# Optimization experiments

Hardware: AMD Instinct MI355X
Metric: run time of the kernel (lower is better)

## Reference

```python
import jax, jax.numpy as jnp
import numpy as np

B, C, W, H, NH, FF, L = 4, 200, 300, 128, 8, 512, 2
PH = H // NH
MAXLEN = 200
PE_N = 512
NEG = -1e15


def _sinusoidal_pe():
    # fairseq-style sinusoidal table, get_embedding(512, hidden_size)
    half = H // 2
    freq = np.exp(np.arange(half, dtype=np.float64) * -(np.log(10000.0) / (half - 1)))
    ang = np.arange(PE_N, dtype=np.float64)[:, None] * freq[None, :]
    return jnp.asarray(np.concatenate([np.sin(ang), np.cos(ang)], axis=1), jnp.float32)

PE = _sinusoidal_pe()  # [512, H], frozen (requires_grad=False in torch)


def setup_inputs() -> dict:
    key = jax.random.key(0)
    ks = jax.random.split(key, 20)

    def lin(k, fan_in, shape):
        lim = 1.0 / np.sqrt(fan_in)
        return jax.random.uniform(k, shape, jnp.float32, -lim, lim)

    return {
        'chars': jax.random.normal(ks[0], (B, C, H), jnp.float32),
        'words': jax.random.normal(ks[1], (B, W, H), jnp.float32),
        'pos_s': jax.random.randint(ks[2], (B, C), 0, MAXLEN),
        'pos_e': jax.random.randint(ks[3], (B, C), 0, MAXLEN),
        'lex_s': jax.random.randint(ks[4], (B, W), 0, MAXLEN),
        'lex_e': jax.random.randint(ks[5], (B, W), 0, MAXLEN),
        'seq_len': jax.random.randint(ks[6], (B,), 100, C + 1),
        'lex_num': jax.random.randint(ks[7], (B,), 150, W + 1),
        # Four_Pos_Fusion 'ff': Linear(4H -> H) + ReLU
        'Wf': lin(ks[8], 4 * H, (4 * H, H)),
        'bf': jnp.zeros((H,), jnp.float32),
        # per-layer attention / FFN params, stacked on leading layer dim
        'Wq': lin(ks[9], H, (L, H, H)),  'bq': jnp.zeros((L, H), jnp.float32),
        'Wk': lin(ks[10], H, (L, H, H)), 'bk': jnp.zeros((L, H), jnp.float32),
        'Wv': lin(ks[11], H, (L, H, H)), 'bv': jnp.zeros((L, H), jnp.float32),
        'Wr': lin(ks[12], H, (L, H, H)), 'br': jnp.zeros((L, H), jnp.float32),
        'u_bias': jax.random.normal(ks[13], (L, NH, PH), jnp.float32) * 0.02,
        'v_bias': jax.random.normal(ks[14], (L, NH, PH), jnp.float32) * 0.02,
        'ln1_g': jnp.ones((L, H), jnp.float32), 'ln1_b': jnp.zeros((L, H), jnp.float32),
        'ln2_g': jnp.ones((L, H), jnp.float32), 'ln2_b': jnp.zeros((L, H), jnp.float32),
        'W1': lin(ks[15], H, (L, H, FF)),  'b1': jnp.zeros((L, FF), jnp.float32),
        'W2': lin(ks[16], FF, (L, FF, H)), 'b2': jnp.zeros((L, H), jnp.float32),
    }


def _ln(x, g, b):
    m = jnp.mean(x, -1, keepdims=True)
    v = jnp.var(x, -1, keepdims=True)
    return (x - m) / jnp.sqrt(v + 1e-5) * g + b


def reference(chars, words, pos_s, pos_e, lex_s, lex_e, seq_len, lex_num,
              Wf, bf, Wq, bq, Wk, bk, Wv, bv, Wr, br, u_bias, v_bias,
              ln1_g, ln1_b, ln2_g, ln2_b, W1, b1, W2, b2):
    # four relative-position distance tables (char span vs word span), offset by max_seq_len
    idx = lambda p, l: jnp.clip(p[:, :, None] - l[:, None, :] + MAXLEN, 0, PE_N - 1)
    # Linear(4H->H) over the concat of four gathered PE tensors, expressed as
    # a sum of 4 chunked matmuls to avoid materializing the [B,C,W,4H] concat.
    rel = (PE[idx(pos_s, lex_s)] @ Wf[0:H] + PE[idx(pos_s, lex_e)] @ Wf[H:2 * H]
           + PE[idx(pos_e, lex_s)] @ Wf[2 * H:3 * H] + PE[idx(pos_e, lex_e)] @ Wf[3 * H:4 * H] + bf)
    rel = jax.nn.relu(rel)  # [B, C, W, H]

    # char_lex_len_to_mask: valid (char i, word j) pairs
    mask = (jnp.arange(C) < seq_len[:, None])[:, :, None] & (jnp.arange(W) < lex_num[:, None])[:, None, :]
    mask = mask[:, None]  # [B, 1, C, W]

    out = chars
    for i in range(L):
        q = (out @ Wq[i] + bq[i]).reshape(B, C, NH, PH)
        k = (words @ Wk[i] + bk[i]).reshape(B, W, NH, PH)
        v = (words @ Wv[i] + bv[i]).reshape(B, W, NH, PH)
        r = (rel @ Wr[i] + br[i]).reshape(B, C, W, NH, PH)
        A_C = jnp.einsum('bcnp,bwnp->bncw', q + u_bias[i], k)
        B_D = jnp.einsum('bcnp,bcwnp->bncw', q + v_bias[i], r)
        score = jnp.where(mask, A_C + B_D, NEG)  # scale=False
        att = jax.nn.softmax(score, axis=-1)
        att = jnp.where(mask, att, 0.0)  # dropout=0 (eval)
        ctx = jnp.einsum('bncw,bwnp->bcnp', att, v).reshape(B, C, H)
        out = _ln(ctx + out, ln1_g[i], ln1_b[i])
        ff = jax.nn.relu(out @ W1[i] + b1[i]) @ W2[i] + b2[i]
        out = _ln(ff + out, ln2_g[i], ln2_b[i])
    return out
```

## Files before the change

kernel.cpp:

```cpp
#include <hip/hip_runtime.h>
#include <math.h>

#define B_ 4
#define C_ 200
#define CH_ 100
#define W_ 300
#define WP_ 304
#define H_ 128
#define NH_ 8
#define PH_ 16
#define FF_ 512
#define L_ 2
#define MAXLEN_ 200
#define PEN_ 512
#define WVS_ 136
#define NTILE_ 19

typedef __bf16 bf16x8 __attribute__((ext_vector_type(8)));
typedef float f32x4v __attribute__((ext_vector_type(4)));

#define SEG_PEW   64
#define SEG_KV    (SEG_PEW + 200)
#define SEG_WR    (SEG_KV + 256)
#define SEG_W1T   (SEG_WR + 128)
#define PREP_BLOCKS (SEG_W1T + 128)

__global__ __launch_bounds__(128) void prep_kernel(
        const float* __restrict__ Wf, const float* __restrict__ bfv,
        const float* __restrict__ words,
        const float* __restrict__ Wk, const float* __restrict__ bk,
        const float* __restrict__ Wv, const float* __restrict__ bv,
        const float* __restrict__ Wr, const float* __restrict__ W1,
        const float* __restrict__ W2,
        __bf16* __restrict__ kb, __bf16* __restrict__ PEWb, __bf16* __restrict__ vTb,
        __bf16* __restrict__ WrB, __bf16* __restrict__ W1T, __bf16* __restrict__ W2T) {
    __shared__ __align__(16) float s_buf[12 * H_];
    __shared__ __align__(16) __bf16 s_vt[128][12];
    __shared__ float s_tile[32][33];
// ... 95 lines not shown
        for (int k = 0; k < 8; ++k) {
            int j = jt * 32 + r + 4 * k;
            s_tile[r + 4 * k][cc] = W1[(l * H_ + j) * FF_ + ut * 32 + cc];
        }
        __syncthreads();
        int jl = t & 31, ul = t >> 5;
        #pragma unroll
        for (int k = 0; k < 8; ++k) {
            int u = ut * 32 + ul + 4 * k;
            W1T[((size_t)(l * FF_ + u)) * H_ + jt * 32 + jl] = (__bf16)s_tile[jl][ul + 4 * k];
        }
    } else {
        int blk = blockIdx.x - SEG_W1T;
        int l = blk >> 6;
        int rem = blk & 63;
        int ut = rem >> 2;
        int ht = rem & 3;
        int r = t >> 5, cc = t & 31;
        #pragma unroll
        for (int k = 0; k < 8; ++k) {
            int u = ut * 32 + r + 4 * k;
            s_tile[r + 4 * k][cc] = W2[(l * FF_ + u) * H_ + ht * 32 + cc];
        }
        __syncthreads();
        int ul = t & 31, hl = t >> 5;
        #pragma unroll
        for (int k = 0; k < 8; ++k) {
            int h = ht * 32 + hl + 4 * k;
            W2T[((size_t)(l * H_ + h)) * FF_ + ut * 32 + ul] = (__bf16)s_tile[ul][hl + 4 * k];
        }
    }
}

__global__ __launch_bounds__(256, 2) void mega_kernel(
    const float* __restrict__ chars,
    const int* __restrict__ pos_s, const int* __restrict__ pos_e,
    const int* __restrict__ lex_s, const int* __restrict__ lex_e,
    const int* __restrict__ seq_len, const int* __restrict__ lex_num,
    const float* __restrict__ Wq, const float* __restrict__ bq,
    const float* __restrict__ br,
    const float* __restrict__ u_bias, const float* __restrict__ v_bias,
    const float* __restrict__ ln1_g, const float* __restrict__ ln1_b,
    const float* __restrict__ ln2_g, const float* __restrict__ ln2_b,
    const float* __restrict__ b1, const float* __restrict__ b2,
    const __bf16* __restrict__ kb, const __bf16* __restrict__ PEWb,
    const __bf16* __restrict__ vTb, const __bf16* __restrict__ WrB,
    const __bf16* __restrict__ W1T, const __bf16* __restrict__ W2T,
    float* __restrict__ out) {

    __shared__ __align__(16) float s_x[2][H_], s_qv[2][H_];
    __shared__ __align__(16) __bf16 s_wvecb[2][16][WVS_];
    __shared__ __align__(16) __bf16 s_qub[2][16][WVS_];
    __shared__ float s_bterm[2][NH_];
    __shared__ __align__(16) float s_sc[2][NH_][WP_];
    __shared__ float s_red[2][132];
    __shared__ __align__(16) float s_hid[2][FF_];
    __shared__ float s_tmp[2][256];
    __shared__ int s_ls[W_], s_le[W_];

    int blk = blockIdx.x;
    int b = blk / CH_, c0 = blk % CH_;
    int t = threadIdx.x;
    int lane = t & 63;
    int wid = t >> 6;
    int l15 = lane & 15, quad = lane >> 4;

    if (t < H_) {
        s_x[0][t] = chars[(b * C_ + c0) * H_ + t];
        s_x[1][t] = chars[(b * C_ + c0 + CH_) * H_ + t];
    }
    for (int w = t; w < W_; w += 256) {
        s_ls[w] = lex_s[b * W_ + w];
        s_le[w] = lex_e[b * W_ + w];
    }
    for (int i = t; i < 2 * 8 * WVS_; i += 256) {
        int r = i / (8 * WVS_), rem = i % (8 * WVS_);
        s_wvecb[r][8 + rem / WVS_][rem % WVS_] = (__bf16)0.f;
    }
    for (int i = t; i < 2 * 16 * WVS_; i += 256) {
        int r = i / (16 * WVS_), rem = i % (16 * WVS_);
        s_qub[r][rem / WVS_][rem % WVS_] = (__bf16)0.f;
    }
    int ps0 = pos_s[b * C_ + c0],        pev0 = pos_e[b * C_ + c0];
    int ps1 = pos_s[b * C_ + c0 + CH_],  pev1 = pos_e[b * C_ + c0 + CH_];
    int slen = seq_len[b];
    int cvalid0 = (c0 < slen), cvalid1 = (c0 + CH_ < slen);
    int wnum = lex_num[b];
    __syncthreads();

    bf16x8 Ac0[5][4], Ac1[5][4];

    #pragma unroll
    for (int li = 0; li < L_; ++li) {
        {
            int half = t >> 7, h = t & 127;
            const float* WqL = Wq + li * H_ * H_;
            const float4* x40 = (const float4*)s_x[0];
            const float4* x41 = (const float4*)s_x[1];
            float4 a0 = {0,0,0,0}, a1 = {0,0,0,0};
            #pragma unroll 2
            for (int g = half * 16; g < half * 16 + 16; ++g) {
                float4 xa = x40[g], xb = x41[g];
                int j0 = 4 * g;
                float w0 = WqL[(j0 + 0) * H_ + h], w1 = WqL[(j0 + 1) * H_ + h];
                float w2 = WqL[(j0 + 2) * H_ + h], w3 = WqL[(j0 + 3) * H_ + h];
                a0.x += xa.x * w0; a0.y += xa.y * w1; a0.z += xa.z * w2; a0.w += xa.w * w3;
                a1.x += xb.x * w0; a1.y += xb.y * w1; a1.z += xb.z * w2; a1.w += xb.w * w3;
            }
            s_tmp[0][t] = (a0.x + a0.y) + (a0.z + a0.w);
            s_tmp[1][t] = (a1.x + a1.y) + (a1.z + a1.w);
        }
        __syncthreads();
        if (t < H_) {
            #pragma unroll
            for (int r = 0; r < 2; ++r) {
                float acc = s_tmp[r][t] + s_tmp[r][t + 128] + bq[li * H_ + t];
                s_qub[r][t >> 4][t] = (__bf16)(acc + u_bias[li * H_ + t]);
                s_qv[r][t] = acc + v_bias[li * H_ + t];
            }
        }
        __syncthreads();

        if (t < H_) {
            const __bf16* WrRow = WrB + li * H_ * H_ + t * H_;
            #pragma unroll 2
            for (int n = 0; n < NH_; ++n) {
                bf16x8 w0 = *(const bf16x8*)(WrRow + n * PH_);
                bf16x8 w1 = *(const bf16x8*)(WrRow + n * PH_ + 8);
                #pragma unroll
                for (int r = 0; r < 2; ++r) {
                    const float4* qv4 = (const float4*)(s_qv[r] + n * PH_);
                    float4 q0 = qv4[0], q1 = qv4[1], q2 = qv4[2], q3 = qv4[3];
                    float4 a4;
                    a4.x = (float)w0[0] * q0.x + (float)w1[0] * q2.x;
                    a4.y = (float)w0[1] * q0.y + (float)w1[1] * q2.y;
                    a4.z = (float)w0[2] * q0.z + (float)w1[2] * q2.z;
                    a4.w = (float)w0[3] * q0.w + (float)w1[3] * q2.w;
                    a4.x += (float)w0[4] * q1.x + (float)w1[4] * q3.x;
                    a4.y += (float)w0[5] * q1.y + (float)w1[5] * q3.y;
                    a4.z += (float)w0[6] * q1.z + (float)w1[6] * q3.z;
                    a4.w += (float)w0[7] * q1.w + (float)w1[7] * q3.w;
                    s_wvecb[r][n][t] = (__bf16)((a4.x + a4.y) + (a4.z + a4.w));
                }
            }
        } else if (t < H_ + NH_) {
            int n = t - H_;
            const float4* br4 = (const float4*)(br + li * H_ + n * PH_);
            float4 b0 = br4[0], b1v = br4[1], b2v = br4[2], b3v = br4[3];
            #pragma unroll
            for (int r = 0; r < 2; ++r) {
                const float4* qv4 = (const float4*)(s_qv[r] + n * PH_);
                float4 q0 = qv4[0], q1 = qv4[1], q2 = qv4[2], q3 = qv4[3];
                float4 a4;
                a4.x = b0.x * q0.x + b2v.x * q2.x;
                a4.y = b0.y * q0.y + b2v.y * q2.y;
                a4.z = b0.z * q0.z + b2v.z * q2.z;
                a4.w = b0.w * q0.w + b2v.w * q2.w;
                a4.x += b1v.x * q1.x + b3v.x * q3.x;
                a4.y += b1v.y * q1.y + b3v.y * q3.y;
                a4.z += b1v.z * q1.z + b3v.z * q3.z;
                a4.w += b1v.w * q1.w + b3v.w * q3.w;
                s_bterm[r][n] = (a4.x + a4.y) + (a4.z + a4.w);
            }
        }
        __syncthreads();

        const __bf16* kL = kb + (size_t)(li * B_ + b) * W_ * H_;
        {
            const __bf16* wrow0 = &s_wvecb[0][l15][0];
            const __bf16* wrow1 = &s_wvecb[1][l15][0];
            const __bf16* qrow0 = &s_qub[0][l15][0];
            const __bf16* qrow1 = &s_qub[1][l15][0];
            #pragma unroll
            for (int tc = 0; tc < 5; ++tc) {
                int tile = wid + 4 * tc;
                if (tile < NTILE_) {
                    int w0t = tile * 16;
                    int w = w0t + l15; if (w > W_ - 1) w = W_ - 1;
                    const __bf16* kr = kL + (size_t)w * H_;
                    f32x4v acc0 = {0.f,0.f,0.f,0.f}, acc1 = {0.f,0.f,0.f,0.f};
                    if (li == 0) {
                        int ls = s_ls[w], le = s_le[w];
                        int i00 = min(max(ps0 - ls + MAXLEN_, 0), PEN_ - 1);
                        int i01 = min(max(ps0 - le + MAXLEN_, 0), PEN_ - 1);
                        int i02 = min(max(pev0 - ls + MAXLEN_, 0), PEN_ - 1);
                        int i03 = min(max(pev0 - le + MAXLEN_, 0), PEN_ - 1);
                        int i10 = min(max(ps1 - ls + MAXLEN_, 0), PEN_ - 1);
                        int i11 = min(max(ps1 - le + MAXLEN_, 0), PEN_ - 1);
                        int i12 = min(max(pev1 - ls + MAXLEN_, 0), PEN_ - 1);
                        int i13 = min(max(pev1 - le + MAXLEN_, 0), PEN_ - 1);
                        const __bf16* r00 = PEWb + (size_t)(0 * PEN_ + i00) * H_;
                        const __bf16* r01 = PEWb + (size_t)(1 * PEN_ + i01) * H_;
                        const __bf16* r02 = PEWb + (size_t)(2 * PEN_ + i02) * H_;
                        const __bf16* r03 = PEWb + (size_t)(3 * PEN_ + i03) * H_;
                        const __bf16* r10 = PEWb + (size_t)(0 * PEN_ + i10) * H_;
                        const __bf16* r11 = PEWb + (size_t)(1 * PEN_ + i11) * H_;
                        const __bf16* r12 = PEWb + (size_t)(2 * PEN_ + i12) * H_;
                        const __bf16* r13 = PEWb + (size_t)(3 * PEN_ + i13) * H_;
                        #pragma unroll
                        for (int s = 0; s < 4; ++s) {
                            int h0 = s * 32 + quad * 8;
                            bf16x8 K = *(const bf16x8*)(kr + h0);
                            bf16x8 A0, A1;
                            {
                                bf16x8 t0 = *(const bf16x8*)(r00 + h0);
                                bf16x8 t1 = *(const bf16x8*)(r01 + h0);
                                bf16x8 t2 = *(const bf16x8*)(r02 + h0);
                                bf16x8 t3 = *(const bf16x8*)(r03 + h0);
                                #pragma unroll
                                for (int j = 0; j < 8; ++j)
                                    A0[j] = (__bf16)fmaxf((float)t0[j] + (float)t1[j] + (float)t2[j] + (float)t3[j], 0.f);
                            }
                            {
                                bf16x8 t0 = *(const bf16x8*)(r10 + h0);
                                bf16x8 t1 = *(const bf16x8*)(r11 + h0);
                                bf16x8 t2 = *(const bf16x8*)(r12 + h0);
                                bf16x8 t3 = *(const bf16x8*)(r13 + h0);
                                #pragma unroll
                                for (int j = 0; j < 8; ++j)
                                    A1[j] = (__bf16)fmaxf((float)t0[j] + (float)t1[j] + (float)t2[j] + (float)t3[j], 0.f);
                            }
                            Ac0[tc][s] = A0;
                            Ac1[tc][s] = A1;
                            bf16x8 Bf0 = *(const bf16x8*)(wrow0 + h0);
                            acc0 = __builtin_amdgcn_mfma_f32_16x16x32_bf16(A0, Bf0, acc0, 0, 0, 0);
                            bf16x8 Bq0 = *(const bf16x8*)(qrow0 + h0);
                            acc0 = __builtin_amdgcn_mfma_f32_16x16x32_bf16(K, Bq0, acc0, 0, 0, 0);
                            bf16x8 Bf1 = *(const bf16x8*)(wrow1 + h0);
                            acc1 = __builtin_amdgcn_mfma_f32_16x16x32_bf16(A1, Bf1, acc1, 0, 0, 0);
                            bf16x8 Bq1 = *(const bf16x8*)(qrow1 + h0);
                            acc1 = __builtin_amdgcn_mfma_f32_16x16x32_bf16(K, Bq1, acc1, 0, 0, 0);
                        }
                    } else {
                        #pragma unroll
                        for (int s = 0; s < 4; ++s) {
                            int h0 = s * 32 + quad * 8;
                            bf16x8 K = *(const bf16x8*)(kr + h0);
                            bf16x8 A0 = Ac0[tc][s];
                            bf16x8 A1 = Ac1[tc][s];
                            bf16x8 Bf0 = *(const bf16x8*)(wrow0 + h0);
                            acc0 = __builtin_amdgcn_mfma_f32_16x16x32_bf16(A0, Bf0, acc0, 0, 0, 0);
                            bf16x8 Bq0 = *(const bf16x8*)(qrow0 + h0);
                            acc0 = __builtin_amdgcn_mfma_f32_16x16x32_bf16(K, Bq0, acc0, 0, 0, 0);
                            bf16x8 Bf1 = *(const bf16x8*)(wrow1 + h0);
                            acc1 = __builtin_amdgcn_mfma_f32_16x16x32_bf16(A1, Bf1, acc1, 0, 0, 0);
                            bf16x8 Bq1 = *(const bf16x8*)(qrow1 + h0);
                            acc1 = __builtin_amdgcn_mfma_f32_16x16x32_bf16(K, Bq1, acc1, 0, 0, 0);
                        }
                    }
                    if (l15 < NH_) {
                        float bt0 = s_bterm[0][l15], bt1 = s_bterm[1][l15];
                        #pragma unroll
                        for (int r = 0; r < 4; ++r) {
                            int wr = w0t + quad * 4 + r;
                            if (wr < W_) {
                                s_sc[0][l15][wr] = acc0[r] + bt0;
                                s_sc[1][l15][wr] = acc1[r] + bt1;
                            }
                        }
                    }
                }
            }
        }
        __syncthreads();

        {
            int n = t >> 5, ln_ = t & 31;
            #pragma unroll
            for (int r = 0; r < 2; ++r) {
                int cval = r ? cvalid1 : cvalid0;
                if (cval) {
                    float m = -INFINITY;
                    for (int w = ln_; w < wnum; w += 32) m = fmaxf(m, s_sc[r][n][w]);
                    #pragma unroll
                    for (int off = 16; off > 0; off >>= 1) m = fmaxf(m, __shfl_xor(m, off, 32));
                    float sum = 0.f;
                    for (int w = ln_; w < wnum; w += 32) sum += expf(s_sc[r][n][w] - m);
                    #pragma unroll
                    for (int off = 16; off > 0; off >>= 1) sum += __shfl_xor(sum, off, 32);
                    float inv = 1.f / sum;
                    for (int w = ln_; w < WP_; w += 32)
                        s_sc[r][n][w] = (w < wnum) ? expf(s_sc[r][n][w] - m) * inv : 0.f;
                } else {
                    for (int w = ln_; w < WP_; w += 32) s_sc[r][n][w] = 0.f;
                }
            }
        }
        __syncthreads();

        {
            int h = t & 127, half = t >> 7, n = h >> 4;
            const __bf16* vrow = vTb + ((size_t)(li * B_ + b) * H_ + h) * WP_;
            const float4* att0 = (const float4*)(s_sc[0][n]);
            const float4* att1 = (const float4*)(s_sc[1][n]);
            float4 a0 = {0,0,0,0}, a1 = {0,0,0,0};
            #pragma unroll 2
            for (int g = half * 19; g < half * 19 + 19; ++g) {
                bf16x8 vv = *(const bf16x8*)(vrow + 8 * g);
                float4 p00 = att0[2 * g], p01 = att0[2 * g + 1];
                float4 p10 = att1[2 * g], p11 = att1[2 * g + 1];
                float v0 = (float)vv[0], v1 = (float)vv[1], v2 = (float)vv[2], v3 = (float)vv[3];
                float v4 = (float)vv[4], v5 = (float)vv[5], v6 = (float)vv[6], v7 = (float)vv[7];
                a0.x += p00.x * v0 + p01.x * v4;
                a0.y += p00.y * v1 + p01.y * v5;
                a0.z += p00.z * v2 + p01.z * v6;
                a0.w += p00.w * v3 + p01.w * v7;
                a1.x += p10.x * v0 + p11.x * v4;
                a1.y += p10.y * v1 + p11.y * v5;
                a1.z += p10.z * v2 + p11.z * v6;
                a1.w += p10.w * v3 + p11.w * v7;
            }
            s_tmp[0][t] = (a0.x + a0.y) + (a0.z + a0.w);
            s_tmp[1][t] = (a1.x + a1.y) + (a1.z + a1.w);
        }
        __syncthreads();

        if (t < 128) {
            s_red[0][t] = s_tmp[0][t] + s_tmp[0][t + 128] + s_x[0][t];
        } else {
            int e = t - 128;
            s_red[1][e] = s_tmp[1][e] + s_tmp[1][e + 128] + s_x[1][e];
        }
        __syncthreads();
        if (t < 128) {
            int r = t >> 6, l = t & 63;
            float a = s_red[r][l], bb = s_red[r][l + 64];
            float s = a + bb, ss = a * a + bb * bb;
            #pragma unroll
            for (int off = 32; off > 0; off >>= 1) {
                s += __shfl_down(s, off);
                ss += __shfl_down(ss, off);
            }
            if (l == 0) {
                float mean = s * (1.f / 128.f);
                float var = ss * (1.f / 128.f) - mean * mean;
                s_red[r][128] = mean;
                s_red[r][129] = rsqrtf(var + 1e-5f);
            }
        }
        __syncthreads();
        if (t < H_) {
            float g1 = ln1_g[li * H_ + t], b1v = ln1_b[li * H_ + t];
            #pragma unroll
            for (int r = 0; r < 2; ++r)
                s_x[r][t] = (s_red[r][t] - s_red[r][128]) * s_red[r][129] * g1 + b1v;
        }
        __syncthreads();

        {
            const __bf16* W1l = W1T + (size_t)li * FF_ * H_;
            int u0 = t * 2;
            const __bf16* ra = W1l + (size_t)u0 * H_;
            const __bf16* rb = W1l + (size_t)(u0 + 1) * H_;
            const float4* x40 = (const float4*)s_x[0];
            const float4* x41 = (const float4*)s_x[1];
            float4 a00 = {0,0,0,0}, a01 = {0,0,0,0}, a10 = {0,0,0,0}, a11 = {0,0,0,0};
            #pragma unroll 2
            for (int g = 0; g < 16; ++g) {
                bf16x8 wa = *(const bf16x8*)(ra + 8 * g);
                bf16x8 wb = *(const bf16x8*)(rb + 8 * g);
                float4 xa0 = x40[2 * g], xa1 = x40[2 * g + 1];
                float4 xb0 = x41[2 * g], xb1 = x41[2 * g + 1];
                a00.x += xa0.x * (float)wa[0] + xa1.x * (float)wa[4];
                a00.y += xa0.y * (float)wa[1] + xa1.y * (float)wa[5];
                a00.z += xa0.z * (float)wa[2] + xa1.z * (float)wa[6];
                a00.w += xa0.w * (float)wa[3] + xa1.w * (float)wa[7];
                a01.x += xa0.x * (float)wb[0] + xa1.x * (float)wb[4];
                a01.y += xa0.y * (float)wb[1] + xa1.y * (float)wb[5];
                a01.z += xa0.z * (float)wb[2] + xa1.z * (float)wb[6];
                a01.w += xa0.w * (float)wb[3] + xa1.w * (float)wb[7];
                a10.x += xb0.x * (float)wa[0] + xb1.x * (float)wa[4];
                a10.y += xb0.y * (float)wa[1] + xb1.y * (float)wa[5];
                a10.z += xb0.z * (float)wa[2] + xb1.z * (float)wa[6];
                a10.w += xb0.w * (float)wa[3] + xb1.w * (float)wa[7];
                a11.x += xb0.x * (float)wb[0] + xb1.x * (float)wb[4];
                a11.y += xb0.y * (float)wb[1] + xb1.y * (float)wb[5];
                a11.z += xb0.z * (float)wb[2] + xb1.z * (float)wb[6];
                a11.w += xb0.w * (float)wb[3] + xb1.w * (float)wb[7];
            }
            float bb0 = b1[li * FF_ + u0], bb1 = b1[li * FF_ + u0 + 1];
            s_hid[0][u0]     = fmaxf((a00.x + a00.y) + (a00.z + a00.w) + bb0, 0.f);
            s_hid[0][u0 + 1] = fmaxf((a01.x + a01.y) + (a01.z + a01.w) + bb1, 0.f);
            s_hid[1][u0]     = fmaxf((a10.x + a10.y) + (a10.z + a10.w) + bb0, 0.f);
            s_hid[1][u0 + 1] = fmaxf((a11.x + a11.y) + (a11.z + a11.w) + bb1, 0.f);
        }
        __syncthreads();

        {
            int half = t >> 7, h = t & 127;
            const __bf16* wrow2 = W2T + ((size_t)li * H_ + h) * FF_ + half * 256;
            const float4* h40 = (const float4*)(s_hid[0] + half * 256);
            const float4* h41 = (const float4*)(s_hid[1] + half * 256);
            float4 a0 = {0,0,0,0}, a1 = {0,0,0,0};
            #pragma unroll 2
            for (int g = 0; g < 32; ++g) {
                bf16x8 wv = *(const bf16x8*)(wrow2 + 8 * g);
                float4 p00 = h40[2 * g], p01 = h40[2 * g + 1];
                float4 p10 = h41[2 * g], p11 = h41[2 * g + 1];
                float v0 = (float)wv[0], v1 = (float)wv[1], v2 = (float)wv[2], v3 = (float)wv[3];
                float v4 = (float)wv[4], v5 = (float)wv[5], v6 = (float)wv[6], v7 = (float)wv[7];
                a0.x += p00.x * v0 + p01.x * v4;
                a0.y += p00.y * v1 + p01.y * v5;
                a0.z += p00.z * v2 + p01.z * v6;
                a0.w += p00.w * v3 + p01.w * v7;
                a1.x += p10.x * v0 + p11.x * v4;
                a1.y += p10.y * v1 + p11.y * v5;
                a1.z += p10.z * v2 + p11.z * v6;
                a1.w += p10.w * v3 + p11.w * v7;
            }
            s_tmp[0][t] = (a0.x + a0.y) + (a0.z + a0.w);
            s_tmp[1][t] = (a1.x + a1.y) + (a1.z + a1.w);
        }
        __syncthreads();

        if (t < 128) {
            s_red[0][t] = s_tmp[0][t] + s_tmp[0][t + 128] + b2[li * H_ + t] + s_x[0][t];
        } else {
            int e = t - 128;
            s_red[1][e] = s_tmp[1][e] + s_tmp[1][e + 128] + b2[li * H_ + e] + s_x[1][e];
        }
        __syncthreads();
        if (t < 128) {
            int r = t >> 6, l = t & 63;
            float a = s_red[r][l], bb = s_red[r][l + 64];
            float s = a + bb, ss = a * a + bb * bb;
            #pragma unroll
            for (int off = 32; off > 0; off >>= 1) {
                s += __shfl_down(s, off);
                ss += __shfl_down(ss, off);
            }
            if (l == 0) {
                float mean = s * (1.f / 128.f);
                float var = ss * (1.f / 128.f) - mean * mean;
                s_red[r][128] = mean;
                s_red[r][129] = rsqrtf(var + 1e-5f);
            }
        }
        __syncthreads();
        if (t < H_) {
            float g2 = ln2_g[li * H_ + t], b2v = ln2_b[li * H_ + t];
            #pragma unroll
            for (int r = 0; r < 2; ++r)
                s_x[r][t] = (s_red[r][t] - s_red[r][128]) * s_red[r][129] * g2 + b2v;
        }
        __syncthreads();
    }

    if (t < H_) {
        out[(b * C_ + c0) * H_ + t] = s_x[0][t];
        out[(b * C_ + c0 + CH_) * H_ + t] = s_x[1][t];
    }
}

extern "C" void kernel_launch(void* const* d_in, const int* in_sizes, int n_in,
                              void* d_out, int out_size, void* d_ws, size_t ws_size,
                              hipStream_t stream) {
    const float* chars  = (const float*)d_in[0];
    const float* words  = (const float*)d_in[1];
    const int* pos_s   = (const int*)d_in[2];
    const int* pos_e   = (const int*)d_in[3];
    const int* lex_s   = (const int*)d_in[4];
    const int* lex_e   = (const int*)d_in[5];
    const int* seq_len = (const int*)d_in[6];
    const int* lex_num = (const int*)d_in[7];
    const float* Wf  = (const float*)d_in[8];
    const float* bfv = (const float*)d_in[9];
    const float* Wq  = (const float*)d_in[10];
    const float* bq  = (const float*)d_in[11];
    const float* Wk  = (const float*)d_in[12];
    const float* bk  = (const float*)d_in[13];
    const float* Wv  = (const float*)d_in[14];
    const float* bv  = (const float*)d_in[15];
    const float* Wr  = (const float*)d_in[16];
    const float* br  = (const float*)d_in[17];
    const float* u_bias = (const float*)d_in[18];
    const float* v_bias = (const float*)d_in[19];
    const float* ln1_g  = (const float*)d_in[20];
    const float* ln1_b  = (const float*)d_in[21];
    const float* ln2_g  = (const float*)d_in[22];
    const float* ln2_b  = (const float*)d_in[23];
    const float* W1  = (const float*)d_in[24];
    const float* b1  = (const float*)d_in[25];
    const float* W2  = (const float*)d_in[26];
    const float* b2  = (const float*)d_in[27];

    __bf16* kb   = (__bf16*)d_ws;
    __bf16* PEWb = kb + (size_t)L_ * B_ * W_ * H_;
    __bf16* vTb  = PEWb + 4 * PEN_ * H_;
    __bf16* WrB  = vTb + (size_t)L_ * B_ * H_ * WP_;
    __bf16* W1T  = WrB + L_ * H_ * H_;
    __bf16* W2T  = W1T + L_ * H_ * FF_;

    prep_kernel<<<dim3(PREP_BLOCKS), dim3(128), 0, stream>>>(
        Wf, bfv, words, Wk, bk, Wv, bv, Wr, W1, W2,
        kb, PEWb, vTb, WrB, W1T, W2T);

    mega_kernel<<<dim3(B_ * CH_), dim3(256), 0, stream>>>(
        chars, pos_s, pos_e, lex_s, lex_e, seq_len, lex_num,
        Wq, bq, br, u_bias, v_bias,
        ln1_g, ln1_b, ln2_g, ln2_b, b1, b2,
        kb, PEWb, vTb, WrB, W1T, W2T, (float*)d_out);
}
```

Baseline: 245.3 us.

## Process four chars per block and recompute rel-pos A tiles each layer

Each block now handles four character rows instead of two, halving the grid to 200 blocks and reusing each loaded weight, key and PE row across four rows. Shared memory moves to a dynamic allocation of about 93 KB, and launch bounds drop to one block per SM. The register cache of layer-0 relative-position A fragments is removed, so the PE gather and ReLU sum are recomputed in every layer to free registers. The cost is fewer blocks for parallelism, since 200 blocks may underfill the GPU's compute units, plus redundant gather work in layer 1.

```diff
diff --git a/kernel.cpp b/kernel.cpp
--- a/kernel.cpp
+++ b/kernel.cpp
@@ -3,7 +3,8 @@
 
 #define B_ 4
 #define C_ 200
-#define CH_ 100
+#define CR_ 50
+#define NR_ 4
 #define W_ 300
 #define WP_ 304
 #define H_ 128
@@ -165,7 +166,8 @@
     }
 }
 
-__global__ __launch_bounds__(256, 2) void mega_kernel(
+#define SMEM_BYTES 94752
+__global__ __launch_bounds__(256, 1) void mega_kernel(
     const float* __restrict__ chars,
     const int* __restrict__ pos_s, const int* __restrict__ pos_e,
     const int* __restrict__ lex_s, const int* __restrict__ lex_e,
@@ -181,72 +183,83 @@
     const __bf16* __restrict__ W1T, const __bf16* __restrict__ W2T,
     float* __restrict__ out) {
 
-    __shared__ __align__(16) float s_x[2][H_], s_qv[2][H_];
-    __shared__ __align__(16) __bf16 s_wvecb[2][16][WVS_];
-    __shared__ __align__(16) __bf16 s_qub[2][16][WVS_];
-    __shared__ float s_bterm[2][NH_];
-    __shared__ __align__(16) float s_sc[2][NH_][WP_];
-    __shared__ float s_red[2][132];
-    __shared__ __align__(16) float s_hid[2][FF_];
-    __shared__ float s_tmp[2][256];
-    __shared__ int s_ls[W_], s_le[W_];
+    extern __shared__ __align__(16) char smem[];
+    float (*s_x)[H_]            = (float (*)[H_])(smem + 0);
+    float (*s_qv)[H_]           = (float (*)[H_])(smem + 2048);
+    __bf16 (*s_wvecb)[16][WVS_] = (__bf16 (*)[16][WVS_])(smem + 4096);
+    __bf16 (*s_qub)[16][WVS_]   = (__bf16 (*)[16][WVS_])(smem + 21504);
+    float (*s_bterm)[NH_]       = (float (*)[NH_])(smem + 38912);
+    float (*s_sc)[NH_][WP_]     = (float (*)[NH_][WP_])(smem + 39040);
+    float (*s_red)[132]         = (float (*)[132])(smem + 77952);
+    float (*s_hid)[FF_]         = (float (*)[FF_])(smem + 80064);
+    float (*s_tmp)[256]         = (float (*)[256])(smem + 88256);
+    int* s_ls                   = (int*)(smem + 92352);
+    int* s_le                   = (int*)(smem + 93552);
 
     int blk = blockIdx.x;
-    int b = blk / CH_, c0 = blk % CH_;
+    int b = blk / CR_, c0 = blk % CR_;
     int t = threadIdx.x;
     int lane = t & 63;
     int wid = t >> 6;
     int l15 = lane & 15, quad = lane >> 4;
 
     if (t < H_) {
-        s_x[0][t] = chars[(b * C_ + c0) * H_ + t];
-        s_x[1][t] = chars[(b * C_ + c0 + CH_) * H_ + t];
+        #pragma unroll
+        for (int r = 0; r < NR_; ++r)
+            s_x[r][t] = chars[(b * C_ + c0 + CR_ * r) * H_ + t];
     }
     for (int w = t; w < W_; w += 256) {
         s_ls[w] = lex_s[b * W_ + w];
         s_le[w] = lex_e[b * W_ + w];
     }
-    for (int i = t; i < 2 * 8 * WVS_; i += 256) {
+    for (int i = t; i < NR_ * 8 * WVS_; i += 256) {
         int r = i / (8 * WVS_), rem = i % (8 * WVS_);
         s_wvecb[r][8 + rem / WVS_][rem % WVS_] = (__bf16)0.f;
     }
-    for (int i = t; i < 2 * 16 * WVS_; i += 256) {
+    for (int i = t; i < NR_ * 16 * WVS_; i += 256) {
         int r = i / (16 * WVS_), rem = i % (16 * WVS_);
         s_qub[r][rem / WVS_][rem % WVS_] = (__bf16)0.f;
     }
-    int ps0 = pos_s[b * C_ + c0],        pev0 = pos_e[b * C_ + c0];
-    int ps1 = pos_s[b * C_ + c0 + CH_],  pev1 = pos_e[b * C_ + c0 + CH_];
+    int ps[NR_], pev[NR_], cval[NR_];
     int slen = seq_len[b];
-    int cvalid0 = (c0 < slen), cvalid1 = (c0 + CH_ < slen);
+    #pragma unroll
+    for (int r = 0; r < NR_; ++r) {
+        int c = c0 + CR_ * r;
+        ps[r]  = pos_s[b * C_ + c];
+        pev[r] = pos_e[b * C_ + c];
+        cval[r] = (c < slen);
+    }
     int wnum = lex_num[b];
     __syncthreads();
 
-    bf16x8 Ac0[5][4], Ac1[5][4];
-
-    #pragma unroll
+    #pragma unroll 1
     for (int li = 0; li < L_; ++li) {
         {
             int half = t >> 7, h = t & 127;
             const float* WqL = Wq + li * H_ * H_;
-            const float4* x40 = (const float4*)s_x[0];
-            const float4* x41 = (const float4*)s_x[1];
-            float4 a0 = {0,0,0,0}, a1 = {0,0,0,0};
+            float4 a[NR_];
+            #pragma unroll
+            for (int r = 0; r < NR_; ++r) a[r] = make_float4(0.f, 0.f, 0.f, 0.f);
             #pragma unroll 2
             for (int g = half * 16; g < half * 16 + 16; ++g) {
-                float4 xa = x40[g], xb = x41[g];
                 int j0 = 4 * g;
                 float w0 = WqL[(j0 + 0) * H_ + h], w1 = WqL[(j0 + 1) * H_ + h];
                 float w2 = WqL[(j0 + 2) * H_ + h], w3 = WqL[(j0 + 3) * H_ + h];
-                a0.x += xa.x * w0; a0.y += xa.y * w1; a0.z += xa.z * w2; a0.w += xa.w * w3;
-                a1.x += xb.x * w0; a1.y += xb.y * w1; a1.z += xb.z * w2; a1.w += xb.w * w3;
-            }
-            s_tmp[0][t] = (a0.x + a0.y) + (a0.z + a0.w);
-            s_tmp[1][t] = (a1.x + a1.y) + (a1.z + a1.w);
+                #pragma unroll
+                for (int r = 0; r < NR_; ++r) {
+                    float4 xa = ((const float4*)s_x[r])[g];
+                    a[r].x += xa.x * w0; a[r].y += xa.y * w1;
+                    a[r].z += xa.z * w2; a[r].w += xa.w * w3;
+                }
+            }
+            #pragma unroll
+            for (int r = 0; r < NR_; ++r)
+                s_tmp[r][t] = (a[r].x + a[r].y) + (a[r].z + a[r].w);
         }
         __syncthreads();
         if (t < H_) {
             #pragma unroll
-            for (int r = 0; r < 2; ++r) {
+            for (int r = 0; r < NR_; ++r) {
                 float acc = s_tmp[r][t] + s_tmp[r][t + 128] + bq[li * H_ + t];
                 s_qub[r][t >> 4][t] = (__bf16)(acc + u_bias[li * H_ + t]);
                 s_qv[r][t] = acc + v_bias[li * H_ + t];
@@ -261,7 +274,7 @@
                 bf16x8 w0 = *(const bf16x8*)(WrRow + n * PH_);
                 bf16x8 w1 = *(const bf16x8*)(WrRow + n * PH_ + 8);
                 #pragma unroll
-                for (int r = 0; r < 2; ++r) {
+                for (int r = 0; r < NR_; ++r) {
                     const float4* qv4 = (const float4*)(s_qv[r] + n * PH_);
                     float4 q0 = qv4[0], q1 = qv4[1], q2 = qv4[2], q3 = qv4[3];
                     float4 a4;
@@ -276,34 +289,26 @@
                     s_wvecb[r][n][t] = (__bf16)((a4.x + a4.y) + (a4.z + a4.w));
                 }
             }
-        } else if (t < H_ + NH_) {
-            int n = t - H_;
-            const float4* br4 = (const float4*)(br + li * H_ + n * PH_);
-            float4 b0 = br4[0], b1v = br4[1], b2v = br4[2], b3v = br4[3];
-            #pragma unroll
-            for (int r = 0; r < 2; ++r) {
-                const float4* qv4 = (const float4*)(s_qv[r] + n * PH_);
-                float4 q0 = qv4[0], q1 = qv4[1], q2 = qv4[2], q3 = qv4[3];
-                float4 a4;
-                a4.x = b0.x * q0.x + b2v.x * q2.x;
-                a4.y = b0.y * q0.y + b2v.y * q2.y;
-                a4.z = b0.z * q0.z + b2v.z * q2.z;
-                a4.w = b0.w * q0.w + b2v.w * q2.w;
-                a4.x += b1v.x * q1.x + b3v.x * q3.x;
-                a4.y += b1v.y * q1.y + b3v.y * q3.y;
-                a4.z += b1v.z * q1.z + b3v.z * q3.z;
-                a4.w += b1v.w * q1.w + b3v.w * q3.w;
-                s_bterm[r][n] = (a4.x + a4.y) + (a4.z + a4.w);
-            }
+        } else if (t < H_ + NR_ * NH_) {
+            int idx = t - H_;
+            int r = idx >> 3, n = idx & 7;
+            float a = 0.f;
+            #pragma unroll
+            for (int k = 0; k < PH_; ++k)
+                a += br[li * H_ + n * PH_ + k] * s_qv[r][n * PH_ + k];
+            s_bterm[r][n] = a;
         }
         __syncthreads();
 
         const __bf16* kL = kb + (size_t)(li * B_ + b) * W_ * H_;
         {
-            const __bf16* wrow0 = &s_wvecb[0][l15][0];
-            const __bf16* wrow1 = &s_wvecb[1][l15][0];
-            const __bf16* qrow0 = &s_qub[0][l15][0];
-            const __bf16* qrow1 = &s_qub[1][l15][0];
+            const __bf16* wrow[NR_];
+            const __bf16* qrow[NR_];
+            #pragma unroll
+            for (int r = 0; r < NR_; ++r) {
+                wrow[r] = &s_wvecb[r][l15][0];
+                qrow[r] = &s_qub[r][l15][0];
+            }
             #pragma unroll
             for (int tc = 0; tc < 5; ++tc) {
                 int tile = wid + 4 * tc;
@@ -311,84 +316,50 @@
                     int w0t = tile * 16;
                     int w = w0t + l15; if (w > W_ - 1) w = W_ - 1;
                     const __bf16* kr = kL + (size_t)w * H_;
-                    f32x4v acc0 = {0.f,0.f,0.f,0.f}, acc1 = {0.f,0.f,0.f,0.f};
-                    if (li == 0) {
-                        int ls = s_ls[w], le = s_le[w];
-                        int i00 = min(max(ps0 - ls + MAXLEN_, 0), PEN_ - 1);
-                        int i01 = min(max(ps0 - le + MAXLEN_, 0), PEN_ - 1);
-                        int i02 = min(max(pev0 - ls + MAXLEN_, 0), PEN_ - 1);
-                        int i03 = min(max(pev0 - le + MAXLEN_, 0), PEN_ - 1);
-                        int i10 = min(max(ps1 - ls + MAXLEN_, 0), PEN_ - 1);
-                        int i11 = min(max(ps1 - le + MAXLEN_, 0), PEN_ - 1);
-                        int i12 = min(max(pev1 - ls + MAXLEN_, 0), PEN_ - 1);
-                        int i13 = min(max(pev1 - le + MAXLEN_, 0), PEN_ - 1);
-                        const __bf16* r00 = PEWb + (size_t)(0 * PEN_ + i00) * H_;
-                        const __bf16* r01 = PEWb + (size_t)(1 * PEN_ + i01) * H_;
-                        const __bf16* r02 = PEWb + (size_t)(2 * PEN_ + i02) * H_;
-                        const __bf16* r03 = PEWb + (size_t)(3 * PEN_ + i03) * H_;
-                        const __bf16* r10 = PEWb + (size_t)(0 * PEN_ + i10) * H_;
-                        const __bf16* r11 = PEWb + (size_t)(1 * PEN_ + i11) * H_;
-                        const __bf16* r12 = PEWb + (size_t)(2 * PEN_ + i12) * H_;
-                        const __bf16* r13 = PEWb + (size_t)(3 * PEN_ + i13) * H_;
+                    int ls = s_ls[w], le = s_le[w];
+                    const __bf16* rp[NR_][4];
+                    #pragma unroll
+                    for (int r = 0; r < NR_; ++r) {
+                        int i0 = min(max(ps[r]  - ls + MAXLEN_, 0), PEN_ - 1);
+                        int i1 = min(max(ps[r]  - le + MAXLEN_, 0), PEN_ - 1);
+                        int i2 = min(max(pev[r] - ls + MAXLEN_, 0), PEN_ - 1);
+                        int i3 = min(max(pev[r] - le + MAXLEN_, 0), PEN_ - 1);
+                        rp[r][0] = PEWb + (size_t)(0 * PEN_ + i0) * H_;
+                        rp[r][1] = PEWb + (size_t)(1 * PEN_ + i1) * H_;
+                        rp[r][2] = PEWb + (size_t)(2 * PEN_ + i2) * H_;
+                        rp[r][3] = PEWb + (size_t)(3 * PEN_ + i3) * H_;
+                    }
+                    f32x4v acc[NR_];
+                    #pragma unroll
+                    for (int r = 0; r < NR_; ++r) acc[r] = (f32x4v){0.f, 0.f, 0.f, 0.f};
+                    #pragma unroll
+                    for (int s = 0; s < 4; ++s) {
+                        int h0 = s * 32 + quad * 8;
+                        bf16x8 K = *(const bf16x8*)(kr + h0);
                         #pragma unroll
-                        for (int s = 0; s < 4; ++s) {
-                            int h0 = s * 32 + quad * 8;
-                            bf16x8 K = *(const bf16x8*)(kr + h0);
-                            bf16x8 A0, A1;
-                            {
-                                bf16x8 t0 = *(const bf16x8*)(r00 + h0);
-                                bf16x8 t1 = *(const bf16x8*)(r01 + h0);
-                                bf16x8 t2 = *(const bf16x8*)(r02 + h0);
-                                bf16x8 t3 = *(const bf16x8*)(r03 + h0);
-                                #pragma unroll
-                                for (int j = 0; j < 8; ++j)
-                                    A0[j] = (__bf16)fmaxf((float)t0[j] + (float)t1[j] + (float)t2[j] + (float)t3[j], 0.f);
-                            }
-                            {
-                                bf16x8 t0 = *(const bf16x8*)(r10 + h0);
-                                bf16x8 t1 = *(const bf16x8*)(r11 + h0);
-                                bf16x8 t2 = *(const bf16x8*)(r12 + h0);
-                                bf16x8 t3 = *(const bf16x8*)(r13 + h0);
-                                #pragma unroll
-                                for (int j = 0; j < 8; ++j)
-                                    A1[j] = (__bf16)fmaxf((float)t0[j] + (float)t1[j] + (float)t2[j] + (float)t3[j], 0.f);
-                            }
-                            Ac0[tc][s] = A0;
-                            Ac1[tc][s] = A1;
-                            bf16x8 Bf0 = *(const bf16x8*)(wrow0 + h0);
-                            acc0 = __builtin_amdgcn_mfma_f32_16x16x32_bf16(A0, Bf0, acc0, 0, 0, 0);
-                            bf16x8 Bq0 = *(const bf16x8*)(qrow0 + h0);
-                            acc0 = __builtin_amdgcn_mfma_f32_16x16x32_bf16(K, Bq0, acc0, 0, 0, 0);
-                            bf16x8 Bf1 = *(const bf16x8*)(wrow1 + h0);
-                            acc1 = __builtin_amdgcn_mfma_f32_16x16x32_bf16(A1, Bf1, acc1, 0, 0, 0);
-                            bf16x8 Bq1 = *(const bf16x8*)(qrow1 + h0);
-                            acc1 = __builtin_amdgcn_mfma_f32_16x16x32_bf16(K, Bq1, acc1, 0, 0, 0);
-                        }
-                    } else {
-                        #pragma unroll
-                        for (int s = 0; s < 4; ++s) {
-                            int h0 = s * 32 + quad * 8;
-                            bf16x8 K = *(const bf16x8*)(kr + h0);
-                            bf16x8 A0 = Ac0[tc][s];
-                            bf16x8 A1 = Ac1[tc][s];
-                            bf16x8 Bf0 = *(const bf16x8*)(wrow0 + h0);
-                            acc0 = __builtin_amdgcn_mfma_f32_16x16x32_bf16(A0, Bf0, acc0, 0, 0, 0);
-                            bf16x8 Bq0 = *(const bf16x8*)(qrow0 + h0);
-                            acc0 = __builtin_amdgcn_mfma_f32_16x16x32_bf16(K, Bq0, acc0, 0, 0, 0);
-                            bf16x8 Bf1 = *(const bf16x8*)(wrow1 + h0);
-                            acc1 = __builtin_amdgcn_mfma_f32_16x16x32_bf16(A1, Bf1, acc1, 0, 0, 0);
-                            bf16x8 Bq1 = *(const bf16x8*)(qrow1 + h0);
-                            acc1 = __builtin_amdgcn_mfma_f32_16x16x32_bf16(K, Bq1, acc1, 0, 0, 0);
+                        for (int r = 0; r < NR_; ++r) {
+                            bf16x8 t0 = *(const bf16x8*)(rp[r][0] + h0);
+                            bf16x8 t1 = *(const bf16x8*)(rp[r][1] + h0);
+                            bf16x8 t2 = *(const bf16x8*)(rp[r][2] + h0);
+                            bf16x8 t3 = *(const bf16x8*)(rp[r][3] + h0);
+                            bf16x8 A;
+                            #pragma unroll
+                            for (int j = 0; j < 8; ++j)
+                                A[j] = (__bf16)fmaxf((float)t0[j] + (float)t1[j] + (float)t2[j] + (float)t3[j], 0.f);
+                            bf16x8 Bf = *(const bf16x8*)(wrow[r] + h0);
+                            acc[r] = __builtin_amdgcn_mfma_f32_16x16x32_bf16(A, Bf, acc[r], 0, 0, 0);
+                            bf16x8 Bq = *(const bf16x8*)(qrow[r] + h0);
+                            acc[r] = __builtin_amdgcn_mfma_f32_16x16x32_bf16(K, Bq, acc[r], 0, 0, 0);
                         }
                     }
                     if (l15 < NH_) {
-                        float bt0 = s_bterm[0][l15], bt1 = s_bterm[1][l15];
                         #pragma unroll
-                        for (int r = 0; r < 4; ++r) {
-                            int wr = w0t + quad * 4 + r;
-                            if (wr < W_) {
-                                s_sc[0][l15][wr] = acc0[r] + bt0;
-                                s_sc[1][l15][wr] = acc1[r] + bt1;
+                        for (int r = 0; r < NR_; ++r) {
+                            float bt = s_bterm[r][l15];
+                            #pragma unroll
+                            for (int q = 0; q < 4; ++q) {
+                                int wr = w0t + quad * 4 + q;
+                                if (wr < W_) s_sc[r][l15][wr] = acc[r][q] + bt;
                             }
                         }
                     }
@@ -400,9 +371,8 @@
         {
             int n = t >> 5, ln_ = t & 31;
             #pragma unroll
-            for (int r = 0; r < 2; ++r) {
-                int cval = r ? cvalid1 : cvalid0;
-                if (cval) {
+            for (int r = 0; r < NR_; ++r) {
+                if (cval[r]) {
                     float m = -INFINITY;
                     for (int w = ln_; w < wnum; w += 32) m = fmaxf(m, s_sc[r][n][w]);
                     #pragma unroll
@@ -424,38 +394,42 @@
         {
             int h = t & 127, half = t >> 7, n = h >> 4;
             const __bf16* vrow = vTb + ((size_t)(li * B_ + b) * H_ + h) * WP_;
-            const float4* att0 = (const float4*)(s_sc[0][n]);
-            const float4* att1 = (const float4*)(s_sc[1][n]);
-            float4 a0 = {0,0,0,0}, a1 = {0,0,0,0};
+            const float4* att[NR_];
+            #pragma unroll
+            for (int r = 0; r < NR_; ++r) att[r] = (const float4*)(s_sc[r][n]);
+            float4 a[NR_];
+            #pragma unroll
+            for (int r = 0; r < NR_; ++r) a[r] = make_float4(0.f, 0.f, 0.f, 0.f);
             #pragma unroll 2
             for (int g = half * 19; g < half * 19 + 19; ++g) {
                 bf16x8 vv = *(const bf16x8*)(vrow + 8 * g);
-                float4 p00 = att0[2 * g], p01 = att0[2 * g + 1];
-                float4 p10 = att1[2 * g], p11 = att1[2 * g + 1];
                 float v0 = (float)vv[0], v1 = (float)vv[1], v2 = (float)vv[2], v3 = (float)vv[3];
                 float v4 = (float)vv[4], v5 = (float)vv[5], v6 = (float)vv[6], v7 = (float)vv[7];
-                a0.x += p00.x * v0 + p01.x * v4;
-                a0.y += p00.y * v1 + p01.y * v5;
-                a0.z += p00.z * v2 + p01.z * v6;
-                a0.w += p00.w * v3 + p01.w * v7;
-                a1.x += p10.x * v0 + p11.x * v4;
-                a1.y += p10.y * v1 + p11.y * v5;
-                a1.z += p10.z * v2 + p11.z * v6;
-                a1.w += p10.w * v3 + p11.w * v7;
-            }
-            s_tmp[0][t] = (a0.x + a0.y) + (a0.z + a0.w);
-            s_tmp[1][t] = (a1.x + a1.y) + (a1.z + a1.w);
-        }
-        __syncthreads();
-
-        if (t < 128) {
-            s_red[0][t] = s_tmp[0][t] + s_tmp[0][t + 128] + s_x[0][t];
-        } else {
-            int e = t - 128;
-            s_red[1][e] = s_tmp[1][e] + s_tmp[1][e + 128] + s_x[1][e];
-        }
-        __syncthreads();
-        if (t < 128) {
+                #pragma unroll
+                for (int r = 0; r < NR_; ++r) {
+                    float4 p0 = att[r][2 * g], p1 = att[r][2 * g + 1];
+                    a[r].x += p0.x * v0 + p1.x * v4;
+                    a[r].y += p0.y * v1 + p1.y * v5;
+                    a[r].z += p0.z * v2 + p1.z * v6;
+                    a[r].w += p0.w * v3 + p1.w * v7;
+                }
+            }
+            #pragma unroll
+            for (int r = 0; r < NR_; ++r)
+                s_tmp[r][t] = (a[r].x + a[r].y) + (a[r].z + a[r].w);
+        }
+        __syncthreads();
+
+        {
+            int rr = t >> 7, e = t & 127;
+            #pragma unroll
+            for (int k = 0; k < 2; ++k) {
+                int r = rr + 2 * k;
+                s_red[r][e] = s_tmp[r][e] + s_tmp[r][e + 128] + s_x[r][e];
+            }
+        }
+        __syncthreads();
+        {
             int r = t >> 6, l = t & 63;
             float a = s_red[r][l], bb = s_red[r][l + 64];
             float s = a + bb, ss = a * a + bb * bb;
@@ -475,7 +449,7 @@
         if (t < H_) {
             float g1 = ln1_g[li * H_ + t], b1v = ln1_b[li * H_ + t];
             #pragma unroll
-            for (int r = 0; r < 2; ++r)
+            for (int r = 0; r < NR_; ++r)
                 s_x[r][t] = (s_red[r][t] - s_red[r][128]) * s_red[r][129] * g1 + b1v;
         }
         __syncthreads();
@@ -484,76 +458,77 @@
             const __bf16* W1l = W1T + (size_t)li * FF_ * H_;
             int u0 = t * 2;
             const __bf16* ra = W1l + (size_t)u0 * H_;
-            const __bf16* rb = W1l + (size_t)(u0 + 1) * H_;
-            const float4* x40 = (const float4*)s_x[0];
-            const float4* x41 = (const float4*)s_x[1];
-            float4 a00 = {0,0,0,0}, a01 = {0,0,0,0}, a10 = {0,0,0,0}, a11 = {0,0,0,0};
+            const __bf16* rb = ra + H_;
+            float4 aA[NR_], aB[NR_];
+            #pragma unroll
+            for (int r = 0; r < NR_; ++r) {
+                aA[r] = make_float4(0.f, 0.f, 0.f, 0.f);
+                aB[r] = make_float4(0.f, 0.f, 0.f, 0.f);
+            }
             #pragma unroll 2
             for (int g = 0; g < 16; ++g) {
                 bf16x8 wa = *(const bf16x8*)(ra + 8 * g);
                 bf16x8 wb = *(const bf16x8*)(rb + 8 * g);
-                float4 xa0 = x40[2 * g], xa1 = x40[2 * g + 1];
-                float4 xb0 = x41[2 * g], xb1 = x41[2 * g + 1];
-                a00.x += xa0.x * (float)wa[0] + xa1.x * (float)wa[4];
-                a00.y += xa0.y * (float)wa[1] + xa1.y * (float)wa[5];
-                a00.z += xa0.z * (float)wa[2] + xa1.z * (float)wa[6];
-                a00.w += xa0.w * (float)wa[3] + xa1.w * (float)wa[7];
-                a01.x += xa0.x * (float)wb[0] + xa1.x * (float)wb[4];
-                a01.y += xa0.y * (float)wb[1] + xa1.y * (float)wb[5];
-                a01.z += xa0.z * (float)wb[2] + xa1.z * (float)wb[6];
-                a01.w += xa0.w * (float)wb[3] + xa1.w * (float)wb[7];
-                a10.x += xb0.x * (float)wa[0] + xb1.x * (float)wa[4];
-                a10.y += xb0.y * (float)wa[1] + xb1.y * (float)wa[5];
-                a10.z += xb0.z * (float)wa[2] + xb1.z * (float)wa[6];
-                a10.w += xb0.w * (float)wa[3] + xb1.w * (float)wa[7];
-                a11.x += xb0.x * (float)wb[0] + xb1.x * (float)wb[4];
-                a11.y += xb0.y * (float)wb[1] + xb1.y * (float)wb[5];
-                a11.z += xb0.z * (float)wb[2] + xb1.z * (float)wb[6];
-                a11.w += xb0.w * (float)wb[3] + xb1.w * (float)wb[7];
+                #pragma unroll
+                for (int r = 0; r < NR_; ++r) {
+                    float4 x0 = ((const float4*)s_x[r])[2 * g];
+                    float4 x1 = ((const float4*)s_x[r])[2 * g + 1];
+                    aA[r].x += x0.x * (float)wa[0] + x1.x * (float)wa[4];
+                    aA[r].y += x0.y * (float)wa[1] + x1.y * (float)wa[5];
+                    aA[r].z += x0.z * (float)wa[2] + x1.z * (float)wa[6];
+                    aA[r].w += x0.w * (float)wa[3] + x1.w * (float)wa[7];
+                    aB[r].x += x0.x * (float)wb[0] + x1.x * (float)wb[4];
+                    aB[r].y += x0.y * (float)wb[1] + x1.y * (float)wb[5];
+                    aB[r].z += x0.z * (float)wb[2] + x1.z * (float)wb[6];
+                    aB[r].w += x0.w * (float)wb[3] + x1.w * (float)wb[7];
+                }
             }
             float bb0 = b1[li * FF_ + u0], bb1 = b1[li * FF_ + u0 + 1];
-            s_hid[0][u0]     = fmaxf((a00.x + a00.y) + (a00.z + a00.w) + bb0, 0.f);
-            s_hid[0][u0 + 1] = fmaxf((a01.x + a01.y) + (a01.z + a01.w) + bb1, 0.f);
-            s_hid[1][u0]     = fmaxf((a10.x + a10.y) + (a10.z + a10.w) + bb0, 0.f);
-            s_hid[1][u0 + 1] = fmaxf((a11.x + a11.y) + (a11.z + a11.w) + bb1, 0.f);
+            #pragma unroll
+            for (int r = 0; r < NR_; ++r) {
+                s_hid[r][u0]     = fmaxf((aA[r].x + aA[r].y) + (aA[r].z + aA[r].w) + bb0, 0.f);
+                s_hid[r][u0 + 1] = fmaxf((aB[r].x + aB[r].y) + (aB[r].z + aB[r].w) + bb1, 0.f);
+            }
         }
         __syncthreads();
 
         {
             int half = t >> 7, h = t & 127;
             const __bf16* wrow2 = W2T + ((size_t)li * H_ + h) * FF_ + half * 256;
-            const float4* h40 = (const float4*)(s_hid[0] + half * 256);
-            const float4* h41 = (const float4*)(s_hid[1] + half * 256);
-            float4 a0 = {0,0,0,0}, a1 = {0,0,0,0};
+            float4 a[NR_];
+            #pragma unroll
+            for (int r = 0; r < NR_; ++r) a[r] = make_float4(0.f, 0.f, 0.f, 0.f);
             #pragma unroll 2
             for (int g = 0; g < 32; ++g) {
                 bf16x8 wv = *(const bf16x8*)(wrow2 + 8 * g);
-                float4 p00 = h40[2 * g], p01 = h40[2 * g + 1];
-                float4 p10 = h41[2 * g], p11 = h41[2 * g + 1];
                 float v0 = (float)wv[0], v1 = (float)wv[1], v2 = (float)wv[2], v3 = (float)wv[3];
                 float v4 = (float)wv[4], v5 = (float)wv[5], v6 = (float)wv[6], v7 = (float)wv[7];
-                a0.x += p00.x * v0 + p01.x * v4;
-                a0.y += p00.y * v1 + p01.y * v5;
-                a0.z += p00.z * v2 + p01.z * v6;
-                a0.w += p00.w * v3 + p01.w * v7;
-                a1.x += p10.x * v0 + p11.x * v4;
-                a1.y += p10.y * v1 + p11.y * v5;
-                a1.z += p10.z * v2 + p11.z * v6;
-                a1.w += p10.w * v3 + p11.w * v7;
-            }
-            s_tmp[0][t] = (a0.x + a0.y) + (a0.z + a0.w);
-            s_tmp[1][t] = (a1.x + a1.y) + (a1.z + a1.w);
-        }
-        __syncthreads();
-
-        if (t < 128) {
-            s_red[0][t] = s_tmp[0][t] + s_tmp[0][t + 128] + b2[li * H_ + t] + s_x[0][t];
-        } else {
-            int e = t - 128;
-            s_red[1][e] = s_tmp[1][e] + s_tmp[1][e + 128] + b2[li * H_ + e] + s_x[1][e];
-        }
-        __syncthreads();
-        if (t < 128) {
+                #pragma unroll
+                for (int r = 0; r < NR_; ++r) {
+                    const float4* h4 = (const float4*)(s_hid[r] + half * 256);
+                    float4 p0 = h4[2 * g], p1 = h4[2 * g + 1];
+                    a[r].x += p0.x * v0 + p1.x * v4;
+                    a[r].y += p0.y * v1 + p1.y * v5;
+                    a[r].z += p0.z * v2 + p1.z * v6;
+                    a[r].w += p0.w * v3 + p1.w * v7;
+                }
+            }
+            #pragma unroll
+            for (int r = 0; r < NR_; ++r)
+                s_tmp[r][t] = (a[r].x + a[r].y) + (a[r].z + a[r].w);
+        }
+        __syncthreads();
+
+        {
+            int rr = t >> 7, e = t & 127;
+            #pragma unroll
+            for (int k = 0; k < 2; ++k) {
+                int r = rr + 2 * k;
+                s_red[r][e] = s_tmp[r][e] + s_tmp[r][e + 128] + b2[li * H_ + e] + s_x[r][e];
+            }
+        }
+        __syncthreads();
+        {
             int r = t >> 6, l = t & 63;
             float a = s_red[r][l], bb = s_red[r][l + 64];
             float s = a + bb, ss = a * a + bb * bb;
@@ -573,15 +548,16 @@
         if (t < H_) {
             float g2 = ln2_g[li * H_ + t], b2v = ln2_b[li * H_ + t];
             #pragma unroll
-            for (int r = 0; r < 2; ++r)
+            for (int r = 0; r < NR_; ++r)
                 s_x[r][t] = (s_red[r][t] - s_red[r][128]) * s_red[r][129] * g2 + b2v;
         }
         __syncthreads();
     }
 
     if (t < H_) {
-        out[(b * C_ + c0) * H_ + t] = s_x[0][t];
-        out[(b * C_ + c0 + CH_) * H_ + t] = s_x[1][t];
+        #pragma unroll
+        for (int r = 0; r < NR_; ++r)
+            out[(b * C_ + c0 + CR_ * r) * H_ + t] = s_x[r][t];
     }
 }
 
@@ -628,7 +604,7 @@
         Wf, bfv, words, Wk, bk, Wv, bv, Wr, W1, W2,
         kb, PEWb, vTb, WrB, W1T, W2T);
 
-    mega_kernel<<<dim3(B_ * CH_), dim3(256), 0, stream>>>(
+    mega_kernel<<<dim3(B_ * CR_), dim3(256), SMEM_BYTES, stream>>>(
         chars, pos_s, pos_e, lex_s, lex_e, seq_len, lex_num,
         Wq, bq, br, u_bias, v_bias,
         ln1_g, ln1_b, ln2_g, ln2_b, b1, b2,
```

After: 273.6 us. 1.12x slower.

## Fuse two character-pair blocks into one 512-thread block sharing lexicon data

Applied to the files above, without the earlier changes.

Each block now runs two independent 256-thread groups, each with its own carved-out region of dynamic shared memory, so the grid shrinks from 400 to 200 blocks. The lexicon start/end arrays are loaded once into shared memory and used by both groups. The aim is to cut per-block setup and redundant global loads. In exchange, every block-wide barrier now ties both groups together, and the smaller grid may leave some compute units idle.

```diff
diff --git a/kernel.cpp b/kernel.cpp
--- a/kernel.cpp
+++ b/kernel.cpp
@@ -3,7 +3,7 @@
 
 #define B_ 4
 #define C_ 200
-#define CH_ 100
+#define CQ_ 50
 #define W_ 300
 #define WP_ 304
 #define H_ 128
@@ -165,7 +165,9 @@
     }
 }
 
-__global__ __launch_bounds__(256, 2) void mega_kernel(
+#define PAIR_BYTES 46176
+#define SMEM_BYTES (2 * PAIR_BYTES + 2400)
+__global__ __launch_bounds__(512, 1) void mega_kernel(
     const float* __restrict__ chars,
     const int* __restrict__ pos_s, const int* __restrict__ pos_e,
     const int* __restrict__ lex_s, const int* __restrict__ lex_e,
@@ -181,28 +183,34 @@
     const __bf16* __restrict__ W1T, const __bf16* __restrict__ W2T,
     float* __restrict__ out) {
 
-    __shared__ __align__(16) float s_x[2][H_], s_qv[2][H_];
-    __shared__ __align__(16) __bf16 s_wvecb[2][16][WVS_];
-    __shared__ __align__(16) __bf16 s_qub[2][16][WVS_];
-    __shared__ float s_bterm[2][NH_];
-    __shared__ __align__(16) float s_sc[2][NH_][WP_];
-    __shared__ float s_red[2][132];
-    __shared__ __align__(16) float s_hid[2][FF_];
-    __shared__ float s_tmp[2][256];
-    __shared__ int s_ls[W_], s_le[W_];
+    extern __shared__ __align__(16) char smem[];
+    int t512 = threadIdx.x;
+    int pair = t512 >> 8;
+    int t = t512 & 255;
+    char* pb = smem + pair * PAIR_BYTES;
+    float (*s_x)[H_]            = (float (*)[H_])(pb + 0);
+    float (*s_qv)[H_]           = (float (*)[H_])(pb + 1024);
+    __bf16 (*s_wvecb)[16][WVS_] = (__bf16 (*)[16][WVS_])(pb + 2048);
+    __bf16 (*s_qub)[16][WVS_]   = (__bf16 (*)[16][WVS_])(pb + 10752);
+    float (*s_bterm)[NH_]       = (float (*)[NH_])(pb + 19456);
+    float (*s_sc)[NH_][WP_]     = (float (*)[NH_][WP_])(pb + 19520);
+    float (*s_red)[132]         = (float (*)[132])(pb + 38976);
+    float (*s_hid)[FF_]         = (float (*)[FF_])(pb + 40032);
+    float (*s_tmp)[256]         = (float (*)[256])(pb + 44128);
+    int* s_ls                   = (int*)(smem + 2 * PAIR_BYTES);
+    int* s_le                   = (int*)(smem + 2 * PAIR_BYTES + 1200);
 
     int blk = blockIdx.x;
-    int b = blk / CH_, c0 = blk % CH_;
-    int t = threadIdx.x;
+    int b = blk / CQ_, c0 = blk % CQ_ + pair * CQ_;
     int lane = t & 63;
     int wid = t >> 6;
     int l15 = lane & 15, quad = lane >> 4;
 
     if (t < H_) {
         s_x[0][t] = chars[(b * C_ + c0) * H_ + t];
-        s_x[1][t] = chars[(b * C_ + c0 + CH_) * H_ + t];
+        s_x[1][t] = chars[(b * C_ + c0 + 100) * H_ + t];
     }
-    for (int w = t; w < W_; w += 256) {
+    for (int w = t512; w < W_; w += 512) {
         s_ls[w] = lex_s[b * W_ + w];
         s_le[w] = lex_e[b * W_ + w];
     }
@@ -214,10 +222,10 @@
         int r = i / (16 * WVS_), rem = i % (16 * WVS_);
         s_qub[r][rem / WVS_][rem % WVS_] = (__bf16)0.f;
     }
-    int ps0 = pos_s[b * C_ + c0],        pev0 = pos_e[b * C_ + c0];
-    int ps1 = pos_s[b * C_ + c0 + CH_],  pev1 = pos_e[b * C_ + c0 + CH_];
+    int ps0 = pos_s[b * C_ + c0],       pev0 = pos_e[b * C_ + c0];
+    int ps1 = pos_s[b * C_ + c0 + 100], pev1 = pos_e[b * C_ + c0 + 100];
     int slen = seq_len[b];
-    int cvalid0 = (c0 < slen), cvalid1 = (c0 + CH_ < slen);
+    int cvalid0 = (c0 < slen), cvalid1 = (c0 + 100 < slen);
     int wnum = lex_num[b];
     __syncthreads();
 
@@ -581,7 +589,7 @@
 
     if (t < H_) {
         out[(b * C_ + c0) * H_ + t] = s_x[0][t];
-        out[(b * C_ + c0 + CH_) * H_ + t] = s_x[1][t];
+        out[(b * C_ + c0 + 100) * H_ + t] = s_x[1][t];
     }
 }
 
@@ -628,7 +636,7 @@
         Wf, bfv, words, Wk, bk, Wv, bv, Wr, W1, W2,
         kb, PEWb, vTb, WrB, W1T, W2T);
 
-    mega_kernel<<<dim3(B_ * CH_), dim3(256), 0, stream>>>(
+    mega_kernel<<<dim3(B_ * CQ_), dim3(512), SMEM_BYTES, stream>>>(
         chars, pos_s, pos_e, lex_s, lex_e, seq_len, lex_num,
         Wq, bq, br, u_bias, v_bias,
         ln1_g, ln1_b, ln2_g, ln2_b, b1, b2,
```

Measured after the change: 250.3 us. +2.0%, slower.
